# Optimization experiments

Measured on AMD Instinct MI355X. Metric: run time of the kernel, lower is better.

The kernel has to match this reference:

```python
import jax, jax.numpy as jnp
import numpy as np

D = 1024  # d_model

# default_syb decomposed statically (forward called with syb=None, pre_train=False):
# rows 0-4:   single nets: net'0' on idx [0,1,2]; net'1' on idx 6; net'2' on idx 6
# rows 5-18:  double net '0' on index pairs below
# rows 19-21: single net '3' on idx [0,1,2]
SINGLE_GROUPS = [(0, [0, 1, 2]), (1, [6]), (2, [6])]  # nets for rows 0-4
DOUBLE_PAIRS = np.array([[0,3],[0,4],[0,5],[0,6],[1,3],[1,4],[1,5],[1,6],
                         [2,3],[2,4],[2,5],[2,6],[4,5],[4,6]])  # rows 5-18
TAIL_SINGLE = (3, [0, 1, 2])  # rows 19-21


def setup_inputs() -> dict:
    key = jax.random.key(0)
    ks = jax.random.split(key, 16)
    bs = 4096
    s = 1.0 / np.sqrt(D)
    feat = jax.random.normal(ks[0], (bs, 7, D), dtype=jnp.float32)
    # 4 single-expert 2-layer MLPs: Linear(D,D) -> ReLU -> Linear(D,2)
    sw1 = jax.random.normal(ks[1], (4, D, D), dtype=jnp.float32) * s
    sb1 = jax.random.normal(ks[2], (4, D), dtype=jnp.float32) * 0.01
    sw2 = jax.random.normal(ks[3], (4, D, 2), dtype=jnp.float32) * s
    sb2 = jax.random.normal(ks[4], (4, 2), dtype=jnp.float32) * 0.01
    # 1 double-expert MLP: Linear(2D,D) -> ReLU -> Linear(D,2)
    dw1 = jax.random.normal(ks[5], (2 * D, D), dtype=jnp.float32) * s
    db1 = jax.random.normal(ks[6], (D,), dtype=jnp.float32) * 0.01
    dw2 = jax.random.normal(ks[7], (D, 2), dtype=jnp.float32) * s
    db2 = jax.random.normal(ks[8], (2,), dtype=jnp.float32) * 0.01
    return {"feat": feat, "sw1": sw1, "sb1": sb1, "sw2": sw2, "sb2": sb2,
            "dw1": dw1, "db1": db1, "dw2": dw2, "db2": db2}


def _mlp(x, w1, b1, w2, b2):
    return jax.nn.relu(x @ w1 + b1) @ w2 + b2


def reference(feat, sw1, sb1, sw2, sb2, dw1, db1, dw2, db2):
    # feat: [B, 7, D] -> out [B, 22, 2], rows ordered as default_syb
    parts = []
    for net, idxs in SINGLE_GROUPS:  # rows 0-4
        g = feat[:, jnp.array(idxs)]                     # [B, n, D]
        parts.append(_mlp(g, sw1[net], sb1[net], sw2[net], sb2[net]))
    i1 = jnp.asarray(DOUBLE_PAIRS[:, 0]); i2 = jnp.asarray(DOUBLE_PAIRS[:, 1])
    pair = jnp.concatenate([feat[:, i1], feat[:, i2]], axis=-1)  # [B, 14, 2D]
    parts.append(_mlp(pair, dw1, db1, dw2, db2))         # rows 5-18
    net, idxs = TAIL_SINGLE                               # rows 19-21
    g = feat[:, jnp.array(idxs)]
    parts.append(_mlp(g, sw1[net], sb1[net], sw2[net], sb2[net]))
    return jnp.concatenate(parts, axis=1)                 # [B, 22, 2]
```

## Files before the change

kernel.cpp:

```cpp
#include <hip/hip_runtime.h>
#include <hip/hip_bf16.h>
#include <stdint.h>


typedef __attribute__((ext_vector_type(4))) float f32x4;
typedef __attribute__((ext_vector_type(8))) short short8;
typedef __attribute__((ext_vector_type(8))) __bf16 bf16x8;

__device__ inline unsigned short f2bf(float f) {
  union { float f; uint32_t u; } x; x.f = f;
  uint32_t u = x.u;
  return (unsigned short)((u + 0x7fffu + ((u >> 16) & 1u)) >> 16);
}

__global__ void init_out(float* __restrict__ out,
                         const float* __restrict__ sb2,
                         const float* __restrict__ db2) {
  int i = blockIdx.x * 256 + threadIdx.x;
  if (i >= 180224) return;
  int c = i & 1;
  int p = (i >> 1) % 22;
  float v;
  if (p < 3)       v = sb2[0 + c];
  else if (p == 3) v = sb2[2 + c];
  else if (p == 4) v = sb2[4 + c];
  else if (p < 19) v = db2[c];
  else             v = sb2[6 + c];
  out[i] = v;
}

__global__ void prep_weights(const float* __restrict__ sw1,
                             const float* __restrict__ dw1,
                             unsigned short* __restrict__ wp) {
  int c = blockIdx.x * 256 + threadIdx.x;
  const float* W;
  size_t ob;
  int local;
  if (c < 524288) {
    int net = c >> 17;
    local = c & 131071;
    W = sw1 + (size_t)net * 1048576;
    ob = (size_t)net * 1048576;
  } else {
    local = c - 524288;
    W = dw1;
    ob = 4194304;
  }
  int c2 = local & 2047;
  int tile = local >> 11;
  int ct = tile & 3;
  int kstep = tile >> 2;
  int kk = c2 >> 10, nblk = (c2 >> 6) & 15, kgrp = (c2 >> 4) & 3, j15 = c2 & 15;
  int kb = kstep * 64 + kk * 32 + kgrp * 8;
  int j = ct * 256 + nblk * 16 + j15;
  short8 v;
#pragma unroll
  for (int e = 0; e < 8; e++) v[e] = (short)f2bf(W[(size_t)(kb + e) * 1024 + j]);
  *(short8*)(wp + ob + (size_t)local * 8) = v;
}

__global__ void prep_feat(const float* __restrict__ feat,
                          unsigned short* __restrict__ fb) {
  int i = blockIdx.x * 256 + threadIdx.x;
  const float* s = feat + (size_t)i * 8;
  f32x4 a = *(const f32x4*)s;
  f32x4 b = *(const f32x4*)(s + 4);
  short8 v;
  v[0] = (short)f2bf(a[0]); v[1] = (short)f2bf(a[1]);
  v[2] = (short)f2bf(a[2]); v[3] = (short)f2bf(a[3]);
  v[4] = (short)f2bf(b[0]); v[5] = (short)f2bf(b[1]);
  v[6] = (short)f2bf(b[2]); v[7] = (short)f2bf(b[3]);
  *(short8*)(fb + (size_t)i * 8) = v;
}

__global__ __launch_bounds__(256) void fused_main(
    const float* __restrict__ sb1, const float* __restrict__ sw2,
    const float* __restrict__ db1, const float* __restrict__ dw2,
    const unsigned short* __restrict__ wp,
    const unsigned short* __restrict__ fb, float* __restrict__ out) {
  __shared__ short8 Abuf0[512];
  __shared__ short8 Abuf1[512];
  __shared__ short8 Bbuf0[2048];
  __shared__ short8 Bbuf1[2048];

  const int tid = threadIdx.x;
  const int lane = tid & 63;
  const int wid = tid >> 6;
  const int r15 = lane & 15;
  const int fr = (lane >> 4) * 16 + r15;

  const int bid = blockIdx.x;
  const int x = bid & 7;
  const int j = bid >> 3;

  int task, nsteps, v;
  const unsigned short* wpt;
  const float* b1;
  const float* w2;
  if (j < 96)       { task = 0; v = x * 96 + j;         wpt = wp;           b1 = sb1;        w2 = sw2;        nsteps = 16; }
  else if (j < 128) { task = 1; v = x * 32 + (j - 96);  wpt = wp + 1048576; b1 = sb1 + 1024; w2 = sw2 + 2048; nsteps = 16; }
  else if (j < 160) { task = 2; v = x * 32 + (j - 128); wpt = wp + 2097152; b1 = sb1 + 2048; w2 = sw2 + 4096; nsteps = 16; }
  else if (j < 608) { task = 3; v = x * 448 + (j - 160); wpt = wp + 4194304; b1 = db1;       w2 = dw2;        nsteps = 32; }
  else              { task = 4; v = x * 96 + (j - 608); wpt = wp + 3145728; b1 = sb1 + 3072; w2 = sw2 + 6144; nsteps = 16; }
  const int ct = v & 3;
  const int rbase = (v >> 2) * 64;

  const unsigned short *p0, *p1;
  {
    int arow = rbase + wid * 16 + r15;
    int ab, as1, as2;
    if (task == 0 || task == 4) {
      ab = arow / 3; int s = arow - ab * 3; as1 = s; as2 = s;
    } else if (task == 3) {
      ab = arow / 14; int pp = arow - ab * 14;
      if (pp < 12) { as1 = pp >> 2; as2 = 3 + (pp & 3); }
      else         { as1 = 4;       as2 = (pp == 12) ? 5 : 6; }
    } else {
      ab = arow; as1 = 6; as2 = 6;
    }
    int kl = (lane >> 4) * 8;
    p0 = fb + ((size_t)ab * 7 + as1) * 1024 + kl;
    p1 = fb + ((size_t)ab * 7 + as2) * 1024 + kl;
  }

  f32x4 acc[4][4] = {};

#define STAGE(KS, AB, BB)                                                     \
  do {                                                                        \
    const int ko_ = ((KS) & 15) * 64;                                         \
    const unsigned short* a_ = ((KS) < 16) ? p0 : p1;                         \
    __builtin_amdgcn_global_load_lds(                                         \
        (const __attribute__((address_space(1))) void*)(a_ + ko_),            \
        (__attribute__((address_space(3))) void*)((char*)(AB) + wid * 1024),  \
        16, 0, 0);                                                            \
    __builtin_amdgcn_global_load_lds(                                         \
        (const __attribute__((address_space(1))) void*)(a_ + ko_ + 32),       \
        (__attribute__((address_space(3))) void*)((char*)(AB) + 4096 + wid * 1024), \
        16, 0, 0);                                                            \
    const unsigned short* ws_ = wpt + (size_t)((KS) * 4 + ct) * 16384;        \
    _Pragma("unroll")                                                         \
    for (int i_ = 0; i_ < 8; i_++) {                                          \
      __builtin_amdgcn_global_load_lds(                                       \
          (const __attribute__((address_space(1))) void*)(ws_ + i_ * 2048 + tid * 8), \
          (__attribute__((address_space(3))) void*)((char*)(BB) + i_ * 4096 + wid * 1024), \
          16, 0, 0);                                                          \
    }                                                                         \
  } while (0)

#define COMPUTE(AB, BB)                                                       \
  do {                                                                        \
    _Pragma("unroll")                                                         \
    for (int kk_ = 0; kk_ < 2; kk_++) {                                       \
      short8 afr[4], bfr[4];                                                  \
      _Pragma("unroll")                                                       \
      for (int m_ = 0; m_ < 4; m_++)                                          \
        afr[m_] = (AB)[kk_ * 256 + m_ * 64 + fr];                             \
      _Pragma("unroll")                                                       \
      for (int n_ = 0; n_ < 4; n_++)                                          \
        bfr[n_] = (BB)[kk_ * 1024 + (wid * 4 + n_) * 64 + fr];                \
      _Pragma("unroll")                                                       \
      for (int m_ = 0; m_ < 4; m_++)                                          \
        _Pragma("unroll")                                                     \
        for (int n_ = 0; n_ < 4; n_++)                                        \
          acc[m_][n_] = __builtin_amdgcn_mfma_f32_16x16x32_bf16(              \
              __builtin_bit_cast(bf16x8, afr[m_]),                            \
              __builtin_bit_cast(bf16x8, bfr[n_]), acc[m_][n_], 0, 0, 0);     \
    }                                                                         \
  } while (0)

  STAGE(0, Abuf0, Bbuf0);
  __syncthreads();

  for (int ks = 0; ks < nsteps; ks += 2) {
    STAGE(ks + 1, Abuf1, Bbuf1);
    COMPUTE(Abuf0, Bbuf0);
    __syncthreads();
    if (ks + 2 < nsteps) STAGE(ks + 2, Abuf0, Bbuf0);
    COMPUTE(Abuf1, Bbuf1);
    __syncthreads();
  }
#undef STAGE
#undef COMPUTE

  float b1v[4], w20v[4], w21v[4];
#pragma unroll
  for (int n = 0; n < 4; n++) {
    int jj = ct * 256 + wid * 64 + n * 16 + r15;
    b1v[n] = b1[jj];
    w20v[n] = w2[2 * jj];
    w21v[n] = w2[2 * jj + 1];
  }
#pragma unroll
  for (int m = 0; m < 4; m++) {
#pragma unroll
    for (int r = 0; r < 4; r++) {
      float s0 = 0.f, s1 = 0.f;
#pragma unroll
      for (int n = 0; n < 4; n++) {
        float h = acc[m][n][r] + b1v[n];
        h = fmaxf(h, 0.f);
        s0 = fmaf(h, w20v[n], s0);
        s1 = fmaf(h, w21v[n], s1);
      }
#pragma unroll
      for (int off = 1; off < 16; off <<= 1) {
        s0 += __shfl_xor(s0, off, 64);
        s1 += __shfl_xor(s1, off, 64);
      }
      if (r15 == 0) {
        int rg = rbase + m * 16 + (lane >> 4) * 4 + r;
        int b, p;
        if (task == 0)      { b = rg / 3;  p = rg - b * 3; }
        else if (task == 1) { b = rg;      p = 3; }
        else if (task == 2) { b = rg;      p = 4; }
        else if (task == 3) { b = rg / 14; p = 5 + (rg - b * 14); }
        else                { b = rg / 3;  p = 19 + (rg - b * 3); }
        atomicAdd(out + ((size_t)b * 44 + p * 2), s0);
        atomicAdd(out + ((size_t)b * 44 + p * 2 + 1), s1);
      }
    }
  }
}

extern "C" void kernel_launch(void* const* d_in, const int* in_sizes, int n_in,
                              void* d_out, int out_size, void* d_ws, size_t ws_size,
                              hipStream_t stream) {
  const float* feat = (const float*)d_in[0];
  const float* sw1  = (const float*)d_in[1];
  const float* sb1  = (const float*)d_in[2];
  const float* sw2  = (const float*)d_in[3];
  const float* sb2  = (const float*)d_in[4];
  const float* dw1  = (const float*)d_in[5];
  const float* db1  = (const float*)d_in[6];
  const float* dw2  = (const float*)d_in[7];
  const float* db2  = (const float*)d_in[8];
  float* out = (float*)d_out;
  unsigned short* wp = (unsigned short*)d_ws;
  unsigned short* fb = wp + 6291456;

  init_out<<<704, 256, 0, stream>>>(out, sb2, db2);
  prep_weights<<<3072, 256, 0, stream>>>(sw1, dw1, wp);
  prep_feat<<<14336, 256, 0, stream>>>(feat, fb);
  fused_main<<<5632, 256, 0, stream>>>(sb1, sw2, db1, dw2, wp, fb, out);
}
```

Before: 547.8 us.

## Restructure double-buffered GEMM loop with explicit vmcnt waits and early prefetch

```diff
diff --git a/kernel.cpp b/kernel.cpp
--- a/kernel.cpp
+++ b/kernel.cpp
@@ -97,11 +97,11 @@
   const unsigned short* wpt;
   const float* b1;
   const float* w2;
-  if (j < 96)       { task = 0; v = x * 96 + j;         wpt = wp;           b1 = sb1;        w2 = sw2;        nsteps = 16; }
-  else if (j < 128) { task = 1; v = x * 32 + (j - 96);  wpt = wp + 1048576; b1 = sb1 + 1024; w2 = sw2 + 2048; nsteps = 16; }
-  else if (j < 160) { task = 2; v = x * 32 + (j - 128); wpt = wp + 2097152; b1 = sb1 + 2048; w2 = sw2 + 4096; nsteps = 16; }
-  else if (j < 608) { task = 3; v = x * 448 + (j - 160); wpt = wp + 4194304; b1 = db1;       w2 = dw2;        nsteps = 32; }
-  else              { task = 4; v = x * 96 + (j - 608); wpt = wp + 3145728; b1 = sb1 + 3072; w2 = sw2 + 6144; nsteps = 16; }
+  if (j < 96)       { task = 0; v = x * 96 + j;          wpt = wp;           b1 = sb1;        w2 = sw2;        nsteps = 16; }
+  else if (j < 128) { task = 1; v = x * 32 + (j - 96);   wpt = wp + 1048576; b1 = sb1 + 1024; w2 = sw2 + 2048; nsteps = 16; }
+  else if (j < 160) { task = 2; v = x * 32 + (j - 128);  wpt = wp + 2097152; b1 = sb1 + 2048; w2 = sw2 + 4096; nsteps = 16; }
+  else if (j < 608) { task = 3; v = x * 448 + (j - 160); wpt = wp + 4194304; b1 = db1;        w2 = dw2;        nsteps = 32; }
+  else              { task = 4; v = x * 96 + (j - 608);  wpt = wp + 3145728; b1 = sb1 + 3072; w2 = sw2 + 6144; nsteps = 16; }
   const int ct = v & 3;
   const int rbase = (v >> 2) * 64;
 
@@ -147,40 +147,46 @@
     }                                                                         \
   } while (0)
 
-#define COMPUTE(AB, BB)                                                       \
+#define HSTEP(T, AB, BB, LAST)                                                \
   do {                                                                        \
+    if (LAST) asm volatile("s_waitcnt vmcnt(0)" ::: "memory");                \
+    else      asm volatile("s_waitcnt vmcnt(10)" ::: "memory");               \
+    __builtin_amdgcn_s_barrier();                                             \
+    short8 afr[2][4], bfr[2][4];                                              \
     _Pragma("unroll")                                                         \
     for (int kk_ = 0; kk_ < 2; kk_++) {                                       \
-      short8 afr[4], bfr[4];                                                  \
       _Pragma("unroll")                                                       \
       for (int m_ = 0; m_ < 4; m_++)                                          \
-        afr[m_] = (AB)[kk_ * 256 + m_ * 64 + fr];                             \
+        afr[kk_][m_] = (AB)[kk_ * 256 + m_ * 64 + fr];                        \
       _Pragma("unroll")                                                       \
       for (int n_ = 0; n_ < 4; n_++)                                          \
-        bfr[n_] = (BB)[kk_ * 1024 + (wid * 4 + n_) * 64 + fr];                \
+        bfr[kk_][n_] = (BB)[kk_ * 1024 + (wid * 4 + n_) * 64 + fr];           \
+    }                                                                         \
+    asm volatile("s_waitcnt lgkmcnt(0)" ::: "memory");                        \
+    __builtin_amdgcn_s_barrier();                                             \
+    if ((T) + 2 < nsteps) STAGE((T) + 2, AB, BB);                             \
+    __builtin_amdgcn_s_setprio(1);                                            \
+    _Pragma("unroll")                                                         \
+    for (int kk_ = 0; kk_ < 2; kk_++)                                         \
       _Pragma("unroll")                                                       \
       for (int m_ = 0; m_ < 4; m_++)                                          \
         _Pragma("unroll")                                                     \
         for (int n_ = 0; n_ < 4; n_++)                                        \
           acc[m_][n_] = __builtin_amdgcn_mfma_f32_16x16x32_bf16(              \
-              __builtin_bit_cast(bf16x8, afr[m_]),                            \
-              __builtin_bit_cast(bf16x8, bfr[n_]), acc[m_][n_], 0, 0, 0);     \
-    }                                                                         \
+              __builtin_bit_cast(bf16x8, afr[kk_][m_]),                       \
+              __builtin_bit_cast(bf16x8, bfr[kk_][n_]), acc[m_][n_], 0, 0, 0);\
+    __builtin_amdgcn_s_setprio(0);                                            \
   } while (0)
 
   STAGE(0, Abuf0, Bbuf0);
-  __syncthreads();
+  STAGE(1, Abuf1, Bbuf1);
 
   for (int ks = 0; ks < nsteps; ks += 2) {
-    STAGE(ks + 1, Abuf1, Bbuf1);
-    COMPUTE(Abuf0, Bbuf0);
-    __syncthreads();
-    if (ks + 2 < nsteps) STAGE(ks + 2, Abuf0, Bbuf0);
-    COMPUTE(Abuf1, Bbuf1);
-    __syncthreads();
+    HSTEP(ks,     Abuf0, Bbuf0, false);
+    HSTEP(ks + 1, Abuf1, Bbuf1, (ks + 2 >= nsteps));
   }
 #undef STAGE
-#undef COMPUTE
+#undef HSTEP
 
   float b1v[4], w20v[4], w21v[4];
 #pragma unroll
```

New measurement: 466.8 us. 1.17x faster.
